# Optimization experiments

Measured on AMD Instinct MI355X. Metric: run time of the kernel, lower is better.

The kernel has to match this reference:

```python
import jax, jax.numpy as jnp
import numpy as np

NUM_LEVEL = 16
LOG_T = 19
TABLE_SIZE = 2 ** LOG_T
FEAT = 2
MIN_RES = 16
MAX_RES = 512
N_POINTS = 262144

# [Teschner et al. 2003] spatial hash primes, wrapped to int32 like torch does
HASH_COEFFS = jnp.asarray(np.array([1, 2654435761, 805459861], dtype=np.uint32).astype(np.int32))


def _resolutions():
    coeff = (MAX_RES / MIN_RES) ** (1.0 / (NUM_LEVEL - 1))
    return jnp.floor(MIN_RES * (jnp.float32(coeff) ** jnp.arange(NUM_LEVEL, dtype=jnp.float32)))


def _spatial_hash(verts_i32):
    # verts_i32: (..., 3) int32; wrap-around int32 multiply then xor, then mod T (non-negative)
    x = HASH_COEFFS * verts_i32
    idx = jnp.bitwise_xor(jnp.bitwise_xor(x[..., 0], x[..., 1]), x[..., 2])
    return jnp.mod(idx, TABLE_SIZE)


def _hash_encode(coords, tables):
    # coords: (N,3) f32 in [0,1); tables: (L,T,F) f16
    res = _resolutions()                                   # (L,)
    scaled = coords[None, :, :] * res[:, None, None]        # (L,N,3)
    floor = jnp.floor(scaled)
    ceil = jnp.ceil(scaled)
    # 8 voxel corners via floor/ceil selection bits
    offs = jnp.asarray(np.array([[(o >> 2) & 1, (o >> 1) & 1, o & 1] for o in range(8)], dtype=np.bool_))
    sel = offs[:, None, None, :]                            # (8,1,1,3)
    corner = jnp.where(sel, ceil[None], floor[None])        # (8,L,N,3)
    comp = jnp.where(sel, floor[None], ceil[None])          # opposite corner (8,L,N,3)
    idx = _spatial_hash(corner.astype(jnp.int32))           # (8,L,N)
    # gather per-level features: tables[l][idx[:,l,:]] -> (L,8,N,F)
    feats = jax.vmap(lambda tab, i: tab[i], in_axes=(0, 1))(tables, idx)
    # trilinear weight of corner o = prod |opposite_corner - scaled|
    w = jnp.prod(jnp.abs(comp - scaled[None]), axis=-1)     # (8,L,N)
    w = jnp.transpose(w, (1, 0, 2))                         # (L,8,N)
    lvl = jnp.sum(feats.astype(jnp.float32) * w[..., None], axis=1)  # (L,N,F)
    return jnp.transpose(lvl, (1, 0, 2)).reshape(coords.shape[0], NUM_LEVEL * FEAT)


def _mlp(x, w_in, b_in, w_h0, b_h0, w_h1, b_h1, w_out, b_out):
    h = jax.nn.relu(x @ w_in.T + b_in)
    h = jax.nn.relu(h @ w_h0.T + b_h0)
    h = jax.nn.relu(h @ w_h1.T + b_h1)
    return h @ w_out.T + b_out


def setup_inputs() -> dict:
    key = jax.random.key(0)
    ks = jax.random.split(key, 8)
    coords = jax.random.uniform(ks[0], (N_POINTS, 3), dtype=jnp.float32)
    tables = (2e-4 * jax.random.uniform(ks[1], (NUM_LEVEL, TABLE_SIZE, FEAT), dtype=jnp.float32) - 1e-4).astype(jnp.float16)
    def lin(k, out_d, in_d):
        return jax.random.normal(k, (out_d, in_d), dtype=jnp.float32) * (1.0 / np.sqrt(in_d))
    return {
        'coords': coords, 'tables': tables,
        'w_in': lin(ks[2], 64, 32), 'b_in': jnp.zeros((64,), jnp.float32),
        'w_h0': lin(ks[3], 64, 64), 'b_h0': jnp.zeros((64,), jnp.float32),
        'w_h1': lin(ks[4], 64, 64), 'b_h1': jnp.zeros((64,), jnp.float32),
        'w_out': lin(ks[5], 16, 64), 'b_out': jnp.zeros((16,), jnp.float32),
    }


def reference(coords, tables, w_in, b_in, w_h0, b_h0, w_h1, b_h1, w_out, b_out):
    enc = _hash_encode(coords, tables)  # (N, 32)
    return _mlp(enc, w_in, b_in, w_h0, b_h0, w_h1, b_h1, w_out, b_out)  # (N, 16)
```

## Files before the change

kernel.cpp:

```cpp
#include <hip/hip_runtime.h>

#define NLVL 16
#define LOGT 19
#define TMASK ((1u << LOGT) - 1u)
#define SCALE 4096.0f
#define INV_SCALE (1.0f / 4096.0f)

typedef _Float16 half_t;
typedef half_t half8 __attribute__((ext_vector_type(8)));
typedef half_t half4 __attribute__((ext_vector_type(4)));
typedef half_t half2v __attribute__((ext_vector_type(2)));
typedef float  float4v __attribute__((ext_vector_type(4)));

__device__ __constant__ float RES_C[NLVL] = {16.f, 20.f, 25.f, 32.f, 40.f, 50.f, 64.f, 80.f,
                                             101.f, 128.f, 161.f, 203.f, 256.f, 322.f, 406.f, 512.f};

__device__ __forceinline__ float4v mfma16(half8 a, half8 b, float4v c) {
    return __builtin_amdgcn_mfma_f32_16x16x32_f16(a, b, c, 0, 0, 0);
}

__global__ __launch_bounds__(256, 8) void nerf_encode_pair(
    const float* __restrict__ coords,
    const float2* __restrict__ tab,
    half_t* __restrict__ encT, int npts)
{
    const int bpl = npts >> 7;
    const int l    = blockIdx.x / bpl;
    const int side = threadIdx.x & 1;
    const int p    = (blockIdx.x % bpl) * 128 + (threadIdx.x >> 1);

    const float cx = coords[p * 3 + 0];
    const float cy = coords[p * 3 + 1];
    const float cz = coords[p * 3 + 2];

    const float r = RES_C[l];
    const float sx = cx * r, sy = cy * r, sz = cz * r;
    const float fx = floorf(sx), fy = floorf(sy), fz = floorf(sz);
    const float gx = ceilf(sx),  gy = ceilf(sy),  gz = ceilf(sz);

    const unsigned hx = side ? (unsigned)(int)gx : (unsigned)(int)fx;
    const float    wx = side ? (sx - fx) : (gx - sx);

    const unsigned hfy = (unsigned)(int)fy * 2654435761u;
    const unsigned hgy = (unsigned)(int)gy * 2654435761u;
    const unsigned hfz = (unsigned)(int)fz * 805459861u;
    const unsigned hgz = (unsigned)(int)gz * 805459861u;

    const float ty = sy - fy, tz = sz - fz;
    const float uy = gy - sy, uz = gz - sz;

    const float2* __restrict__ base = tab + (((unsigned)l) << LOGT);

    const unsigned i0 = (hx ^ hfy ^ hfz) & TMASK;  const float w0 = wx * uy * uz;
    const unsigned i1 = (hx ^ hfy ^ hgz) & TMASK;  const float w1 = wx * uy * tz;
    const unsigned i2 = (hx ^ hgy ^ hfz) & TMASK;  const float w2 = wx * ty * uz;
    const unsigned i3 = (hx ^ hgy ^ hgz) & TMASK;  const float w3 = wx * ty * tz;

    const float2 v0 = base[i0];
    const float2 v1 = base[i1];
    const float2 v2 = base[i2];
    const float2 v3 = base[i3];

    float e0 = w0 * v0.x + w1 * v1.x + w2 * v2.x + w3 * v3.x;
    float e1 = w0 * v0.y + w1 * v1.y + w2 * v2.y + w3 * v3.y;

    e0 += __shfl_xor(e0, 1, 64);
    e1 += __shfl_xor(e1, 1, 64);

    if (side == 0) {
        half2v hv;
        hv[0] = (half_t)(e0 * SCALE);
        hv[1] = (half_t)(e1 * SCALE);
        *reinterpret_cast<half2v*>(&encT[((size_t)l * npts + p) * 2]) = hv;
    }
}

__global__ __launch_bounds__(256, 2) void nerf_mlp(
    const half_t* __restrict__ encT,
    const float* __restrict__ w_in, const float* __restrict__ b_in,
    const float* __restrict__ w_h0, const float* __restrict__ b_h0,
    const float* __restrict__ w_h1, const float* __restrict__ b_h1,
    const float* __restrict__ w_out, const float* __restrict__ b_out,
    float* __restrict__ out, int npts)
{
    __shared__ half_t actS[4][2][32 * 64];

    const int t    = threadIdx.x;
    const int lane = t & 63;
    const int wv   = t >> 6;
    const int m    = lane & 15;
    const int quad = lane >> 4;

    auto loadA = [&](const float* __restrict__ W, int ncol, int row, int col) -> half8 {
        const float* p = W + row * ncol + col;
        const float4v lo = *reinterpret_cast<const float4v*>(p);
        const float4v hi = *reinterpret_cast<const float4v*>(p + 4);
        half8 r;
        r[0] = (half_t)lo[0]; r[1] = (half_t)lo[1]; r[2] = (half_t)lo[2]; r[3] = (half_t)lo[3];
        r[4] = (half_t)hi[0]; r[5] = (half_t)hi[1]; r[6] = (half_t)hi[2]; r[7] = (half_t)hi[3];
        return r;
    };

    half8 aL1[4], aL2[8], aL3[8], aL4[2];
    #pragma unroll
    for (int mt = 0; mt < 4; ++mt) aL1[mt] = loadA(w_in, 32, mt * 16 + m, quad * 8);
    #pragma unroll
    for (int mt = 0; mt < 4; ++mt) {
        aL2[mt * 2 + 0] = loadA(w_h0, 64, mt * 16 + m, 0 * 32 + quad * 8);
        aL2[mt * 2 + 1] = loadA(w_h0, 64, mt * 16 + m, 1 * 32 + quad * 8);
        aL3[mt * 2 + 0] = loadA(w_h1, 64, mt * 16 + m, 0 * 32 + quad * 8);
        aL3[mt * 2 + 1] = loadA(w_h1, 64, mt * 16 + m, 1 * 32 + quad * 8);
    }
    aL4[0] = loadA(w_out, 64, m, 0 * 32 + quad * 8);
    aL4[1] = loadA(w_out, 64, m, 1 * 32 + quad * 8);

    float4v bL1[4], bL2[4], bL3[4], bL4;
    #pragma unroll
    for (int mt = 0; mt < 4; ++mt) {
        bL1[mt] = *reinterpret_cast<const float4v*>(b_in + mt * 16 + quad * 4);
        bL2[mt] = *reinterpret_cast<const float4v*>(b_h0 + mt * 16 + quad * 4);
        bL3[mt] = *reinterpret_cast<const float4v*>(b_h1 + mt * 16 + quad * 4);
    }
    bL4 = *reinterpret_cast<const float4v*>(b_out + quad * 4);

    half_t* const ping = &actS[wv][0][0];
    half_t* const pong = &actS[wv][1][0];
    const float4v zero = {0.f, 0.f, 0.f, 0.f};

    auto storeTile = [&](half_t* buf, int lp, int mt, float4v acc, float4v bias) {
        half4 h4;
        #pragma unroll
        for (int r = 0; r < 4; ++r)
            h4[r] = (half_t)fmaxf(fmaf(bias[r], SCALE, acc[r]), 0.f);
        const int c16  = mt * 2 + (quad >> 1);
        const int phys = c16 ^ (lp & 7);
        *reinterpret_cast<half4*>(&buf[lp * 64 + phys * 8 + (quad & 1) * 4]) = h4;
    };
    auto loadB = [&](const half_t* buf, int lp, int h) -> half8 {
        const int phys = (h * 4 + quad) ^ (lp & 7);
        return *reinterpret_cast<const half8*>(&buf[lp * 64 + phys * 8]);
    };

    for (int g = 0; g < 2; ++g) {
        #pragma unroll
        for (int nt = 0; nt < 2; ++nt) {
            const int lp  = nt * 16 + m;
            const size_t ptg = (size_t)blockIdx.x * 256 + (size_t)wv * 64 + g * 32 + lp;

            half8 be;
            #pragma unroll
            for (int d = 0; d < 4; ++d) {
                const int L = quad * 4 + d;
                const half2v v = *reinterpret_cast<const half2v*>(&encT[((size_t)L * npts + ptg) * 2]);
                be[d * 2 + 0] = v[0];
                be[d * 2 + 1] = v[1];
            }
            #pragma unroll
            for (int mt = 0; mt < 4; ++mt) {
                float4v acc = mfma16(aL1[mt], be, zero);
                storeTile(ping, lp, mt, acc, bL1[mt]);
            }

            {
                const half8 p0 = loadB(ping, lp, 0);
                const half8 p1 = loadB(ping, lp, 1);
                #pragma unroll
                for (int mt = 0; mt < 4; ++mt) {
                    float4v acc = mfma16(aL2[mt * 2 + 0], p0, zero);
                    acc         = mfma16(aL2[mt * 2 + 1], p1, acc);
                    storeTile(pong, lp, mt, acc, bL2[mt]);
                }
            }

            {
                const half8 p0 = loadB(pong, lp, 0);
                const half8 p1 = loadB(pong, lp, 1);
                #pragma unroll
                for (int mt = 0; mt < 4; ++mt) {
                    float4v acc = mfma16(aL3[mt * 2 + 0], p0, zero);
                    acc         = mfma16(aL3[mt * 2 + 1], p1, acc);
                    storeTile(ping, lp, mt, acc, bL3[mt]);
                }
            }

            {
                const half8 p0 = loadB(ping, lp, 0);
                const half8 p1 = loadB(ping, lp, 1);
                float4v acc = mfma16(aL4[0], p0, zero);
                acc         = mfma16(aL4[1], p1, acc);
                float4v res;
                #pragma unroll
                for (int r = 0; r < 4; ++r)
                    res[r] = fmaf(acc[r], INV_SCALE, bL4[r]);
                *reinterpret_cast<float4v*>(out + ptg * 16 + quad * 4) = res;
            }
        }
    }
}

__global__ __launch_bounds__(256, 2) void nerf_fused(
    const float* __restrict__ coords,
    const float2* __restrict__ tab,
    const float* __restrict__ w_in, const float* __restrict__ b_in,
    const float* __restrict__ w_h0, const float* __restrict__ b_h0,
    const float* __restrict__ w_h1, const float* __restrict__ b_h1,
    const float* __restrict__ w_out, const float* __restrict__ b_out,
    float* __restrict__ out, int npts)
{
    __shared__ half_t encS[256 * 40];
    __shared__ half_t actS[4][2][32 * 64];

    const int t    = threadIdx.x;
    const int lane = t & 63;
    const int wv   = t >> 6;
    const int m    = lane & 15;
    const int quad = lane >> 4;
    const int pt = blockIdx.x * 256 + t;

    {
        const float cx = coords[pt * 3 + 0];
        const float cy = coords[pt * 3 + 1];
        const float cz = coords[pt * 3 + 2];
        float enc[32];
        #pragma unroll
        for (int l = 0; l < NLVL; ++l) {
            const float r = RES_C[l];
            const float sx = cx * r, sy = cy * r, sz = cz * r;
            const float fx = floorf(sx), fy = floorf(sy), fz = floorf(sz);
            const float gx = ceilf(sx),  gy = ceilf(sy),  gz = ceilf(sz);
            const unsigned hfx = (unsigned)(int)fx;
            const unsigned hgx = (unsigned)(int)gx;
            const unsigned hfy = (unsigned)(int)fy * 2654435761u;
            const unsigned hgy = (unsigned)(int)gy * 2654435761u;
            const unsigned hfz = (unsigned)(int)fz * 805459861u;
            const unsigned hgz = (unsigned)(int)gz * 805459861u;
            const float tx = sx - fx, ty = sy - fy, tz = sz - fz;
            const float ux = gx - sx, uy = gy - sy, uz = gz - sz;
            const unsigned lbase = ((unsigned)l) << LOGT;
            float e0 = 0.f, e1 = 0.f;
            #pragma unroll
            for (int o = 0; o < 8; ++o) {
                const unsigned h = ((o & 4) ? hgx : hfx)
                                 ^ ((o & 2) ? hgy : hfy)
                                 ^ ((o & 1) ? hgz : hfz);
                const unsigned idx = h & TMASK;
                const float w = (((o & 4) ? tx : ux)
                              *  ((o & 2) ? ty : uy))
                              *  ((o & 1) ? tz : uz);
                const float2 fv = tab[lbase + idx];
                e0 = fmaf(w, fv.x, e0);
                e1 = fmaf(w, fv.y, e1);
            }
            enc[2 * l + 0] = e0;
            enc[2 * l + 1] = e1;
        }
        #pragma unroll
        for (int c = 0; c < 4; ++c) {
            half8 h8;
            #pragma unroll
            for (int j = 0; j < 8; ++j) h8[j] = (half_t)(enc[c * 8 + j] * SCALE);
            *reinterpret_cast<half8*>(&encS[t * 40 + c * 8]) = h8;
        }
    }

    auto loadA = [&](const float* __restrict__ W, int ncol, int row, int col) -> half8 {
        const float* p = W + row * ncol + col;
        const float4v lo = *reinterpret_cast<const float4v*>(p);
        const float4v hi = *reinterpret_cast<const float4v*>(p + 4);
        half8 r;
        r[0] = (half_t)lo[0]; r[1] = (half_t)lo[1]; r[2] = (half_t)lo[2]; r[3] = (half_t)lo[3];
        r[4] = (half_t)hi[0]; r[5] = (half_t)hi[1]; r[6] = (half_t)hi[2]; r[7] = (half_t)hi[3];
        return r;
    };

    half8 aL1[4], aL2[8], aL3[8], aL4[2];
    #pragma unroll
    for (int mt = 0; mt < 4; ++mt) aL1[mt] = loadA(w_in, 32, mt * 16 + m, quad * 8);
    #pragma unroll
    for (int mt = 0; mt < 4; ++mt) {
        aL2[mt * 2 + 0] = loadA(w_h0, 64, mt * 16 + m, 0 * 32 + quad * 8);
        aL2[mt * 2 + 1] = loadA(w_h0, 64, mt * 16 + m, 1 * 32 + quad * 8);
        aL3[mt * 2 + 0] = loadA(w_h1, 64, mt * 16 + m, 0 * 32 + quad * 8);
        aL3[mt * 2 + 1] = loadA(w_h1, 64, mt * 16 + m, 1 * 32 + quad * 8);
    }
    aL4[0] = loadA(w_out, 64, m, 0 * 32 + quad * 8);
    aL4[1] = loadA(w_out, 64, m, 1 * 32 + quad * 8);

    float4v bL1[4], bL2[4], bL3[4], bL4;
    #pragma unroll
    for (int mt = 0; mt < 4; ++mt) {
        bL1[mt] = *reinterpret_cast<const float4v*>(b_in + mt * 16 + quad * 4);
        bL2[mt] = *reinterpret_cast<const float4v*>(b_h0 + mt * 16 + quad * 4);
        bL3[mt] = *reinterpret_cast<const float4v*>(b_h1 + mt * 16 + quad * 4);
    }
    bL4 = *reinterpret_cast<const float4v*>(b_out + quad * 4);

    half_t* const ping = &actS[wv][0][0];
    half_t* const pong = &actS[wv][1][0];
    const float4v zero = {0.f, 0.f, 0.f, 0.f};

    auto storeTile = [&](half_t* buf, int lp, int mt, float4v acc, float4v bias) {
        half4 h4;
        #pragma unroll
        for (int r = 0; r < 4; ++r)
            h4[r] = (half_t)fmaxf(fmaf(bias[r], SCALE, acc[r]), 0.f);
        const int c16  = mt * 2 + (quad >> 1);
        const int phys = c16 ^ (lp & 7);
        *reinterpret_cast<half4*>(&buf[lp * 64 + phys * 8 + (quad & 1) * 4]) = h4;
    };
    auto loadB = [&](const half_t* buf, int lp, int h) -> half8 {
        const int phys = (h * 4 + quad) ^ (lp & 7);
        return *reinterpret_cast<const half8*>(&buf[lp * 64 + phys * 8]);
    };

    for (int g = 0; g < 2; ++g) {
        #pragma unroll
        for (int nt = 0; nt < 2; ++nt) {
            const int lp   = nt * 16 + m;
            const int prow = wv * 64 + g * 32 + lp;
            const half8 be = *reinterpret_cast<const half8*>(&encS[prow * 40 + quad * 8]);
            #pragma unroll
            for (int mt = 0; mt < 4; ++mt) {
                float4v acc = mfma16(aL1[mt], be, zero);
                storeTile(ping, lp, mt, acc, bL1[mt]);
            }
            {
                const half8 p0 = loadB(ping, lp, 0);
                const half8 p1 = loadB(ping, lp, 1);
                #pragma unroll
                for (int mt = 0; mt < 4; ++mt) {
                    float4v acc = mfma16(aL2[mt * 2 + 0], p0, zero);
                    acc         = mfma16(aL2[mt * 2 + 1], p1, acc);
                    storeTile(pong, lp, mt, acc, bL2[mt]);
                }
            }
            {
                const half8 p0 = loadB(pong, lp, 0);
                const half8 p1 = loadB(pong, lp, 1);
                #pragma unroll
                for (int mt = 0; mt < 4; ++mt) {
                    float4v acc = mfma16(aL3[mt * 2 + 0], p0, zero);
                    acc         = mfma16(aL3[mt * 2 + 1], p1, acc);
                    storeTile(ping, lp, mt, acc, bL3[mt]);
                }
            }
            {
                const half8 p0 = loadB(ping, lp, 0);
                const half8 p1 = loadB(ping, lp, 1);
                float4v acc = mfma16(aL4[0], p0, zero);
                acc         = mfma16(aL4[1], p1, acc);
                float4v res;
                #pragma unroll
                for (int r = 0; r < 4; ++r)
                    res[r] = fmaf(acc[r], INV_SCALE, bL4[r]);
                const size_t ptg = (size_t)blockIdx.x * 256 + (size_t)wv * 64 + g * 32 + lp;
                *reinterpret_cast<float4v*>(out + ptg * 16 + quad * 4) = res;
            }
        }
    }
}

extern "C" void kernel_launch(void* const* d_in, const int* in_sizes, int n_in,
                              void* d_out, int out_size, void* d_ws, size_t ws_size,
                              hipStream_t stream) {
    const float*  coords = (const float*)d_in[0];
    const float2* tables = (const float2*)d_in[1];
    const float*  w_in   = (const float*)d_in[2];
    const float*  b_in   = (const float*)d_in[3];
    const float*  w_h0   = (const float*)d_in[4];
    const float*  b_h0   = (const float*)d_in[5];
    const float*  w_h1   = (const float*)d_in[6];
    const float*  b_h1   = (const float*)d_in[7];
    const float*  w_out  = (const float*)d_in[8];
    const float*  b_out  = (const float*)d_in[9];
    float* out = (float*)d_out;

    const int npts = in_sizes[0] / 3;
    const size_t encBytes = (size_t)npts * 32 * sizeof(half_t);

    if (ws_size >= encBytes && (npts & 255) == 0) {
        half_t* encT = (half_t*)d_ws;
        const int bpl = npts >> 7;
        nerf_encode_pair<<<bpl * NLVL, 256, 0, stream>>>(coords, tables, encT, npts);
        nerf_mlp<<<npts / 256, 256, 0, stream>>>(encT,
                                                 w_in, b_in, w_h0, b_h0,
                                                 w_h1, b_h1, w_out, b_out,
                                                 out, npts);
    } else {
        nerf_fused<<<npts / 256, 256, 0, stream>>>(coords, tables,
                                                   w_in, b_in, w_h0, b_h0,
                                                   w_h1, b_h1, w_out, b_out,
                                                   out, npts);
    }
}
```

Before: 220.1 us.

## Process two points per thread in encoder and batch MLP tiles per wave

The encode kernel now handles two points per thread pair, so eight independent hash-table gathers are in flight per thread and the block count is halved. The MLP kernel loads all four 16-point encoding tiles up front and runs each layer across the four tiles before moving to the next layer, which doubles the per-wave shared activation buffers. The aim is more memory-level parallelism on the random gathers and the encoding loads, plus more independent MFMA work between LDS round-trips. The cost is higher register pressure and twice the LDS per block, which may reduce occupancy.

```diff
diff --git a/kernel.cpp b/kernel.cpp
--- a/kernel.cpp
+++ b/kernel.cpp
@@ -19,63 +19,75 @@
     return __builtin_amdgcn_mfma_f32_16x16x32_f16(a, b, c, 0, 0, 0);
 }
 
-__global__ __launch_bounds__(256, 8) void nerf_encode_pair(
+__global__ __launch_bounds__(256, 8) void nerf_encode_pair2(
     const float* __restrict__ coords,
     const float2* __restrict__ tab,
     half_t* __restrict__ encT, int npts)
 {
-    const int bpl = npts >> 7;
+    const int bpl  = npts >> 8;
     const int l    = blockIdx.x / bpl;
     const int side = threadIdx.x & 1;
-    const int p    = (blockIdx.x % bpl) * 128 + (threadIdx.x >> 1);
-
-    const float cx = coords[p * 3 + 0];
-    const float cy = coords[p * 3 + 1];
-    const float cz = coords[p * 3 + 2];
+    const int base = (blockIdx.x % bpl) * 256 + (threadIdx.x >> 1);
+    const int p0 = base, p1 = base + 128;
 
     const float r = RES_C[l];
-    const float sx = cx * r, sy = cy * r, sz = cz * r;
-    const float fx = floorf(sx), fy = floorf(sy), fz = floorf(sz);
-    const float gx = ceilf(sx),  gy = ceilf(sy),  gz = ceilf(sz);
-
-    const unsigned hx = side ? (unsigned)(int)gx : (unsigned)(int)fx;
-    const float    wx = side ? (sx - fx) : (gx - sx);
-
-    const unsigned hfy = (unsigned)(int)fy * 2654435761u;
-    const unsigned hgy = (unsigned)(int)gy * 2654435761u;
-    const unsigned hfz = (unsigned)(int)fz * 805459861u;
-    const unsigned hgz = (unsigned)(int)gz * 805459861u;
-
-    const float ty = sy - fy, tz = sz - fz;
-    const float uy = gy - sy, uz = gz - sz;
-
-    const float2* __restrict__ base = tab + (((unsigned)l) << LOGT);
-
-    const unsigned i0 = (hx ^ hfy ^ hfz) & TMASK;  const float w0 = wx * uy * uz;
-    const unsigned i1 = (hx ^ hfy ^ hgz) & TMASK;  const float w1 = wx * uy * tz;
-    const unsigned i2 = (hx ^ hgy ^ hfz) & TMASK;  const float w2 = wx * ty * uz;
-    const unsigned i3 = (hx ^ hgy ^ hgz) & TMASK;  const float w3 = wx * ty * tz;
-
-    const float2 v0 = base[i0];
-    const float2 v1 = base[i1];
-    const float2 v2 = base[i2];
-    const float2 v3 = base[i3];
-
-    float e0 = w0 * v0.x + w1 * v1.x + w2 * v2.x + w3 * v3.x;
-    float e1 = w0 * v0.y + w1 * v1.y + w2 * v2.y + w3 * v3.y;
-
-    e0 += __shfl_xor(e0, 1, 64);
-    e1 += __shfl_xor(e1, 1, 64);
+    const float2* __restrict__ bp = tab + (((unsigned)l) << LOGT);
+
+    const float ax = coords[p0 * 3 + 0] * r, ay = coords[p0 * 3 + 1] * r, az = coords[p0 * 3 + 2] * r;
+    const float afx = floorf(ax), afy = floorf(ay), afz = floorf(az);
+    const float agx = ceilf(ax),  agy = ceilf(ay),  agz = ceilf(az);
+    const unsigned ahx = side ? (unsigned)(int)agx : (unsigned)(int)afx;
+    const float    awx = side ? (ax - afx) : (agx - ax);
+    const unsigned ahfy = (unsigned)(int)afy * 2654435761u;
+    const unsigned ahgy = (unsigned)(int)agy * 2654435761u;
+    const unsigned ahfz = (unsigned)(int)afz * 805459861u;
+    const unsigned ahgz = (unsigned)(int)agz * 805459861u;
+    const float aty = ay - afy, atz = az - afz, auy = agy - ay, auz = agz - az;
+
+    const float bx = coords[p1 * 3 + 0] * r, by = coords[p1 * 3 + 1] * r, bz = coords[p1 * 3 + 2] * r;
+    const float bfx = floorf(bx), bfy = floorf(by), bfz = floorf(bz);
+    const float bgx = ceilf(bx),  bgy = ceilf(by),  bgz = ceilf(bz);
+    const unsigned bhx = side ? (unsigned)(int)bgx : (unsigned)(int)bfx;
+    const float    bwx = side ? (bx - bfx) : (bgx - bx);
+    const unsigned bhfy = (unsigned)(int)bfy * 2654435761u;
+    const unsigned bhgy = (unsigned)(int)bgy * 2654435761u;
+    const unsigned bhfz = (unsigned)(int)bfz * 805459861u;
+    const unsigned bhgz = (unsigned)(int)bgz * 805459861u;
+    const float bty = by - bfy, btz = bz - bfz, buy = bgy - by, buz = bgz - bz;
+
+    const float2 a0 = bp[(ahx ^ ahfy ^ ahfz) & TMASK];
+    const float2 a1 = bp[(ahx ^ ahfy ^ ahgz) & TMASK];
+    const float2 a2 = bp[(ahx ^ ahgy ^ ahfz) & TMASK];
+    const float2 a3 = bp[(ahx ^ ahgy ^ ahgz) & TMASK];
+    const float2 b0 = bp[(bhx ^ bhfy ^ bhfz) & TMASK];
+    const float2 b1 = bp[(bhx ^ bhfy ^ bhgz) & TMASK];
+    const float2 b2 = bp[(bhx ^ bhgy ^ bhfz) & TMASK];
+    const float2 b3 = bp[(bhx ^ bhgy ^ bhgz) & TMASK];
+
+    const float aw0 = awx * auy * auz, aw1 = awx * auy * atz;
+    const float aw2 = awx * aty * auz, aw3 = awx * aty * atz;
+    const float bw0 = bwx * buy * buz, bw1 = bwx * buy * btz;
+    const float bw2 = bwx * bty * buz, bw3 = bwx * bty * btz;
+
+    float ae0 = aw0 * a0.x + aw1 * a1.x + aw2 * a2.x + aw3 * a3.x;
+    float ae1 = aw0 * a0.y + aw1 * a1.y + aw2 * a2.y + aw3 * a3.y;
+    float be0 = bw0 * b0.x + bw1 * b1.x + bw2 * b2.x + bw3 * b3.x;
+    float be1 = bw0 * b0.y + bw1 * b1.y + bw2 * b2.y + bw3 * b3.y;
+
+    ae0 += __shfl_xor(ae0, 1, 64);
+    ae1 += __shfl_xor(ae1, 1, 64);
+    be0 += __shfl_xor(be0, 1, 64);
+    be1 += __shfl_xor(be1, 1, 64);
 
     if (side == 0) {
-        half2v hv;
-        hv[0] = (half_t)(e0 * SCALE);
-        hv[1] = (half_t)(e1 * SCALE);
-        *reinterpret_cast<half2v*>(&encT[((size_t)l * npts + p) * 2]) = hv;
+        half2v h0; h0[0] = (half_t)(ae0 * SCALE); h0[1] = (half_t)(ae1 * SCALE);
+        half2v h1; h1[0] = (half_t)(be0 * SCALE); h1[1] = (half_t)(be1 * SCALE);
+        *reinterpret_cast<half2v*>(&encT[((size_t)l * npts + p0) * 2]) = h0;
+        *reinterpret_cast<half2v*>(&encT[((size_t)l * npts + p1) * 2]) = h1;
     }
 }
 
-__global__ __launch_bounds__(256, 2) void nerf_mlp(
+__global__ __launch_bounds__(256, 2) void nerf_mlp4(
     const half_t* __restrict__ encT,
     const float* __restrict__ w_in, const float* __restrict__ b_in,
     const float* __restrict__ w_h0, const float* __restrict__ b_h0,
@@ -83,13 +95,28 @@
     const float* __restrict__ w_out, const float* __restrict__ b_out,
     float* __restrict__ out, int npts)
 {
-    __shared__ half_t actS[4][2][32 * 64];
+    __shared__ half_t actS[4][2][64 * 64];
 
     const int t    = threadIdx.x;
     const int lane = t & 63;
     const int wv   = t >> 6;
     const int m    = lane & 15;
     const int quad = lane >> 4;
+
+    const size_t pbase = (size_t)blockIdx.x * 256 + (size_t)wv * 64;
+
+    half8 be[4];
+    #pragma unroll
+    for (int T = 0; T < 4; ++T) {
+        #pragma unroll
+        for (int d = 0; d < 4; ++d) {
+            const int L = quad * 4 + d;
+            const half2v v = *reinterpret_cast<const half2v*>(
+                &encT[((size_t)L * npts + pbase + T * 16 + m) * 2]);
+            be[T][d * 2 + 0] = v[0];
+            be[T][d * 2 + 1] = v[1];
+        }
+    }
 
     auto loadA = [&](const float* __restrict__ W, int ncol, int row, int col) -> half8 {
         const float* p = W + row * ncol + col;
@@ -141,60 +168,54 @@
         return *reinterpret_cast<const half8*>(&buf[lp * 64 + phys * 8]);
     };
 
-    for (int g = 0; g < 2; ++g) {
-        #pragma unroll
-        for (int nt = 0; nt < 2; ++nt) {
-            const int lp  = nt * 16 + m;
-            const size_t ptg = (size_t)blockIdx.x * 256 + (size_t)wv * 64 + g * 32 + lp;
-
-            half8 be;
-            #pragma unroll
-            for (int d = 0; d < 4; ++d) {
-                const int L = quad * 4 + d;
-                const half2v v = *reinterpret_cast<const half2v*>(&encT[((size_t)L * npts + ptg) * 2]);
-                be[d * 2 + 0] = v[0];
-                be[d * 2 + 1] = v[1];
-            }
-            #pragma unroll
-            for (int mt = 0; mt < 4; ++mt) {
-                float4v acc = mfma16(aL1[mt], be, zero);
-                storeTile(ping, lp, mt, acc, bL1[mt]);
-            }
-
-            {
-                const half8 p0 = loadB(ping, lp, 0);
-                const half8 p1 = loadB(ping, lp, 1);
-                #pragma unroll
-                for (int mt = 0; mt < 4; ++mt) {
-                    float4v acc = mfma16(aL2[mt * 2 + 0], p0, zero);
-                    acc         = mfma16(aL2[mt * 2 + 1], p1, acc);
-                    storeTile(pong, lp, mt, acc, bL2[mt]);
-                }
-            }
-
-            {
-                const half8 p0 = loadB(pong, lp, 0);
-                const half8 p1 = loadB(pong, lp, 1);
-                #pragma unroll
-                for (int mt = 0; mt < 4; ++mt) {
-                    float4v acc = mfma16(aL3[mt * 2 + 0], p0, zero);
-                    acc         = mfma16(aL3[mt * 2 + 1], p1, acc);
-                    storeTile(ping, lp, mt, acc, bL3[mt]);
-                }
-            }
-
-            {
-                const half8 p0 = loadB(ping, lp, 0);
-                const half8 p1 = loadB(ping, lp, 1);
-                float4v acc = mfma16(aL4[0], p0, zero);
-                acc         = mfma16(aL4[1], p1, acc);
-                float4v res;
-                #pragma unroll
-                for (int r = 0; r < 4; ++r)
-                    res[r] = fmaf(acc[r], INV_SCALE, bL4[r]);
-                *reinterpret_cast<float4v*>(out + ptg * 16 + quad * 4) = res;
-            }
-        }
+    #pragma unroll
+    for (int T = 0; T < 4; ++T) {
+        const int lp = T * 16 + m;
+        #pragma unroll
+        for (int mt = 0; mt < 4; ++mt) {
+            float4v acc = mfma16(aL1[mt], be[T], zero);
+            storeTile(ping, lp, mt, acc, bL1[mt]);
+        }
+    }
+
+    #pragma unroll
+    for (int T = 0; T < 4; ++T) {
+        const int lp = T * 16 + m;
+        const half8 p0 = loadB(ping, lp, 0);
+        const half8 p1 = loadB(ping, lp, 1);
+        #pragma unroll
+        for (int mt = 0; mt < 4; ++mt) {
+            float4v acc = mfma16(aL2[mt * 2 + 0], p0, zero);
+            acc         = mfma16(aL2[mt * 2 + 1], p1, acc);
+            storeTile(pong, lp, mt, acc, bL2[mt]);
+        }
+    }
+
+    #pragma unroll
+    for (int T = 0; T < 4; ++T) {
+        const int lp = T * 16 + m;
+        const half8 p0 = loadB(pong, lp, 0);
+        const half8 p1 = loadB(pong, lp, 1);
+        #pragma unroll
+        for (int mt = 0; mt < 4; ++mt) {
+            float4v acc = mfma16(aL3[mt * 2 + 0], p0, zero);
+            acc         = mfma16(aL3[mt * 2 + 1], p1, acc);
+            storeTile(ping, lp, mt, acc, bL3[mt]);
+        }
+    }
+
+    #pragma unroll
+    for (int T = 0; T < 4; ++T) {
+        const int lp = T * 16 + m;
+        const half8 p0 = loadB(ping, lp, 0);
+        const half8 p1 = loadB(ping, lp, 1);
+        float4v acc = mfma16(aL4[0], p0, zero);
+        acc         = mfma16(aL4[1], p1, acc);
+        float4v res;
+        #pragma unroll
+        for (int r = 0; r < 4; ++r)
+            res[r] = fmaf(acc[r], INV_SCALE, bL4[r]);
+        *reinterpret_cast<float4v*>(out + (pbase + lp) * 16 + quad * 4) = res;
     }
 }
 
@@ -318,10 +339,10 @@
         for (int nt = 0; nt < 2; ++nt) {
             const int lp   = nt * 16 + m;
             const int prow = wv * 64 + g * 32 + lp;
-            const half8 be = *reinterpret_cast<const half8*>(&encS[prow * 40 + quad * 8]);
+            const half8 bfr = *reinterpret_cast<const half8*>(&encS[prow * 40 + quad * 8]);
             #pragma unroll
             for (int mt = 0; mt < 4; ++mt) {
-                float4v acc = mfma16(aL1[mt], be, zero);
+                float4v acc = mfma16(aL1[mt], bfr, zero);
                 storeTile(ping, lp, mt, acc, bL1[mt]);
             }
             {
@@ -380,12 +401,12 @@
 
     if (ws_size >= encBytes && (npts & 255) == 0) {
         half_t* encT = (half_t*)d_ws;
-        const int bpl = npts >> 7;
-        nerf_encode_pair<<<bpl * NLVL, 256, 0, stream>>>(coords, tables, encT, npts);
-        nerf_mlp<<<npts / 256, 256, 0, stream>>>(encT,
-                                                 w_in, b_in, w_h0, b_h0,
-                                                 w_h1, b_h1, w_out, b_out,
-                                                 out, npts);
+        const int bpl = npts >> 8;
+        nerf_encode_pair2<<<bpl * NLVL, 256, 0, stream>>>(coords, tables, encT, npts);
+        nerf_mlp4<<<npts / 256, 256, 0, stream>>>(encT,
+                                                  w_in, b_in, w_h0, b_h0,
+                                                  w_h1, b_h1, w_out, b_out,
+                                                  out, npts);
     } else {
         nerf_fused<<<npts / 256, 256, 0, stream>>>(coords, tables,
                                                    w_in, b_in, w_h0, b_h0,
```

Result: no change. 221.1 us (+0.4%).
